# Kernel optimization log

Hardware: AMD Instinct MI355X
Metric: run time of the kernel (lower is better)

The kernel has to match this reference:

```python
import jax, jax.numpy as jnp
import numpy as np

E = 64       # expert_nums
D = 32       # embed_dim
H = 4        # num_heads
HD = D // H  # head_dim = 8
B = 524288
TOP_K = 2
NOISE_EPS = 0.01


def setup_inputs() -> dict:
    key = jax.random.key(0)
    ks = jax.random.split(key, 10)
    return {
        "taskID": jax.random.randint(ks[0], (B,), 0, 6),
        "embed_table": jax.random.normal(ks[1], (6, D), jnp.float32),
        "expert_keys": jax.random.normal(ks[2], (D, D), jnp.float32),
        "in_proj_w": jax.random.normal(ks[3], (3 * D, D), jnp.float32) * 0.1,
        "in_proj_b": jax.random.normal(ks[4], (3 * D,), jnp.float32) * 0.1,
        "fc_gate_w": jax.random.normal(ks[5], (E, D), jnp.float32) * 0.1,
        "fc_gate_b": jax.random.normal(ks[6], (E,), jnp.float32) * 0.1,
        "fc_noise_w": jax.random.normal(ks[7], (E, D), jnp.float32) * 0.1,
        "fc_noise_b": jax.random.normal(ks[8], (E,), jnp.float32) * 0.1,
        "noise": jax.random.normal(ks[9], (B, E), jnp.float32),
    }


def reference(taskID, embed_table, expert_keys, in_proj_w, in_proj_b,
              fc_gate_w, fc_gate_b, fc_noise_w, fc_noise_b, noise):
    bsz = taskID.shape[0]
    x = embed_table[taskID]                                   # [B, D] task embeddings (query)
    # nn.MultiheadAttention q/k projections (v and out_proj don't affect attn_weights)
    Wq, Wk = in_proj_w[:D], in_proj_w[D:2 * D]
    bq, bk = in_proj_b[:D], in_proj_b[D:2 * D]
    Q = (x @ Wq.T + bq).reshape(bsz, H, HD)                   # [B, H, HD]
    K = (expert_keys @ Wk.T + bk).reshape(D, H, HD)           # [S=32, H, HD], shared across batch
    scores = jnp.einsum('bhd,shd->bhs', Q, K) / np.sqrt(HD).astype(np.float32)
    attn_w = jax.nn.softmax(scores, axis=-1).mean(axis=1)     # averaged over heads -> [B, 32]
    expert_weight = jax.nn.softmax(attn_w, axis=-1)           # module re-applies softmax (faithful)
    clean_logits = expert_weight @ fc_gate_w.T + fc_gate_b    # [B, E]
    noise_std = jax.nn.softplus(expert_weight @ fc_noise_w.T + fc_noise_b) + NOISE_EPS
    logits = clean_logits + noise * noise_std                 # train=True path
    top_logits, top_indices = jax.lax.top_k(logits, min(TOP_K + 1, E))
    tk_logits = top_logits[:, :TOP_K]                         # [B, TOP_K]
    tk_indices = top_indices[:, :TOP_K]
    tk_gates = jax.nn.softmax(tk_logits, axis=-1)
    rows = jnp.arange(bsz)[:, None]
    gates = jnp.zeros_like(logits).at[rows, tk_indices].set(tk_gates)  # scatter sparse gates
    load = gates.sum(axis=0)                                  # [E]
    return gates, load
```

## Files before the change

### kernel.cpp

```cpp
#include <hip/hip_runtime.h>
#include <math.h>

#define NE 64
#define NTASK 6
#define BLK 256
#define GRID 1024
#define RPI 32

__global__ void precompute_kernel(
    const float* __restrict__ embed_table,
    const float* __restrict__ expert_keys,
    const float* __restrict__ in_proj_w,
    const float* __restrict__ in_proj_b,
    const float* __restrict__ fc_gate_w,
    const float* __restrict__ fc_gate_b,
    const float* __restrict__ fc_noise_w,
    const float* __restrict__ fc_noise_b,
    float*   __restrict__ tab_f,
    double2* __restrict__ tab_d,
    float*   __restrict__ load)
{
    __shared__ double Ksh[32][32];
    __shared__ double Qsh[6][32];
    __shared__ double sc[24][32];
    __shared__ double attn[6][32];
    __shared__ double ew[6][32];
    __shared__ double red[24];
    __shared__ double red2[6];
    const int tid = threadIdx.x;

    if (tid < NE) load[tid] = 0.f;

    for (int idx = tid; idx < 32 * 32; idx += BLK) {
        int s = idx >> 5, j = idx & 31;
        double acc = (double)in_proj_b[32 + j];
        for (int d = 0; d < 32; ++d)
            acc += (double)expert_keys[s * 32 + d] * (double)in_proj_w[(32 + j) * 32 + d];
        Ksh[s][j] = acc;
    }
    for (int idx = tid; idx < NTASK * 32; idx += BLK) {
        int t = idx >> 5, j = idx & 31;
        double acc = (double)in_proj_b[j];
        for (int d = 0; d < 32; ++d)
            acc += (double)embed_table[t * 32 + d] * (double)in_proj_w[j * 32 + d];
        Qsh[t][j] = acc;
    }
    __syncthreads();

    const double SCALE = 1.0 / (double)((float)2.8284271247461903);
    for (int idx = tid; idx < 24 * 32; idx += BLK) {
        int th = idx >> 5, s = idx & 31;
        int t = th >> 2, h = th & 3;
        double acc = 0.0;
        for (int d = 0; d < 8; ++d)
            acc += Qsh[t][h * 8 + d] * Ksh[s][h * 8 + d];
        sc[th][s] = acc * SCALE;
    }
    __syncthreads();
    if (tid < 24) {
        double m = sc[tid][0];
        for (int s = 1; s < 32; ++s) m = fmax(m, sc[tid][s]);
        red[tid] = m;
    }
    __syncthreads();
    for (int idx = tid; idx < 24 * 32; idx += BLK) {
        int th = idx >> 5, s = idx & 31;
        sc[th][s] = exp(sc[th][s] - red[th]);
    }
    __syncthreads();
    if (tid < 24) {
        double sum = 0.0;
        for (int s = 0; s < 32; ++s) sum += sc[tid][s];
        red[tid] = 1.0 / sum;
    }
    __syncthreads();
    for (int idx = tid; idx < NTASK * 32; idx += BLK) {
        int t = idx >> 5, s = idx & 31;
        attn[t][s] = 0.25 * (sc[t*4+0][s]*red[t*4+0] + sc[t*4+1][s]*red[t*4+1]
                           + sc[t*4+2][s]*red[t*4+2] + sc[t*4+3][s]*red[t*4+3]);
    }
    __syncthreads();
    if (tid < NTASK) {
        double m = attn[tid][0];
        for (int s = 1; s < 32; ++s) m = fmax(m, attn[tid][s]);
        red2[tid] = m;
    }
    __syncthreads();
    for (int idx = tid; idx < NTASK * 32; idx += BLK) {
        int t = idx >> 5, s = idx & 31;
        ew[t][s] = exp(attn[t][s] - red2[t]);
    }
    __syncthreads();
    if (tid < NTASK) {
        double sum = 0.0;
        for (int s = 0; s < 32; ++s) sum += ew[tid][s];
        red2[tid] = 1.0 / sum;
    }
    __syncthreads();

    for (int idx = tid; idx < NTASK * NE; idx += BLK) {
        int t = idx >> 6, e = idx & 63;
        double inv = red2[t];
        double a  = (double)fc_gate_b[e];
        double n0 = (double)fc_noise_b[e];
        for (int d = 0; d < 32; ++d) {
            double w = ew[t][d] * inv;
            a  += w * (double)fc_gate_w [e * 32 + d];
            n0 += w * (double)fc_noise_w[e * 32 + d];
        }
        double sp = (n0 > 0.0) ? (n0 + log1p(exp(-n0))) : log1p(exp(n0));
        double ns = sp + 0.01;
        const int o = t * 64 + e;
        tab_f[o * 2 + 0] = (float)a;
        tab_f[o * 2 + 1] = (float)ns;
        tab_d[o] = make_double2(a, ns);
    }
    for (int idx = tid; idx < 512; idx += BLK) {
        if ((idx >> 6) >= NTASK) {
            tab_f[idx * 2 + 0] = 0.f;
            tab_f[idx * 2 + 1] = 0.f;
            tab_d[idx] = make_double2(0.0, 0.0);
        }
    }
}

__global__ __launch_bounds__(BLK) void router_kernel(
    const int*     __restrict__ taskID,
    const float4*  __restrict__ noise4,
    const float4*  __restrict__ tabf4,
    const double2* __restrict__ tabd,
    float4* __restrict__ gates4,
    float*  __restrict__ load,
    int B)
{
    __shared__ float4  s_tabf4[256];
    __shared__ double2 s_tabd[512];
    __shared__ float   s_load[NE];

    const int tid = threadIdx.x;
    for (int i = tid; i < 256; i += BLK) {
        const int tt = i >> 5, cc = (i >> 3) & 3, rr = i & 7;
        const int dst = (i & ~7) | (rr ^ ((2 * cc + tt) & 7));
        s_tabf4[dst] = tabf4[i];
    }
    for (int i = tid; i < 512; i += BLK) s_tabd[i] = tabd[i];
    if (tid < NE) s_load[tid] = 0.f;
    __syncthreads();

    const int lane  = tid & 63;
    const int sub   = lane >> 2;
    const int c     = lane & 3;
    const int ebase = c * 16;
    const int W = (blockIdx.x * BLK + tid) >> 6;
    const int nWaves = GRID * (BLK / 64);
    const int nGroup = (B + RPI - 1) / RPI;

    int   tcA = 0, tcB = 0;
    float4 a0, a1, a2, a3, a4, a5, a6, a7;
    a0=a1=a2=a3=a4=a5=a6=a7 = make_float4(0.f,0.f,0.f,0.f);
    bool okA = false, okB = false;
    int  rowA = 0, rowB = 0;

    if (W < nGroup) {
        rowA = W * RPI + sub;       okA = rowA < B;
        rowB = W * RPI + 16 + sub;  okB = rowB < B;
        if (okA) {
            tcA = taskID[rowA];
            const int nb = rowA * 16 + c * 4;
            a0 = noise4[nb+0]; a1 = noise4[nb+1]; a2 = noise4[nb+2]; a3 = noise4[nb+3];
        }
        if (okB) {
            tcB = taskID[rowB];
            const int nb = rowB * 16 + c * 4;
            a4 = noise4[nb+0]; a5 = noise4[nb+1]; a6 = noise4[nb+2]; a7 = noise4[nb+3];
        }
    }

    for (int g = W; g < nGroup; g += nWaves) {
        const int gn = g + nWaves;
        int   tnA = 0, tnB = 0;
        float4 b0, b1, b2, b3, b4, b5, b6, b7;
        b0=b1=b2=b3=b4=b5=b6=b7 = make_float4(0.f,0.f,0.f,0.f);
        bool oknA = false, oknB = false;
        int  rownA = 0, rownB = 0;
        if (gn < nGroup) {
            rownA = gn * RPI + sub;       oknA = rownA < B;
            rownB = gn * RPI + 16 + sub;  oknB = rownB < B;
            if (oknA) {
                tnA = taskID[rownA];
                const int nb = rownA * 16 + c * 4;
                b0 = noise4[nb+0]; b1 = noise4[nb+1]; b2 = noise4[nb+2]; b3 = noise4[nb+3];
            }
            if (oknB) {
                tnB = taskID[rownB];
                const int nb = rownB * 16 + c * 4;
                b4 = noise4[nb+0]; b5 = noise4[nb+1]; b6 = noise4[nb+2]; b7 = noise4[nb+3];
            }
        }

#define INS(l_, e_, n_) {                                                      \
        const bool b1_ = (l_) > v1, b2_ = (l_) > v2, b3_ = (l_) > v3;          \
        v3 = b2_ ? v2 : (b3_ ? (l_) : v3);                                     \
        i3 = b2_ ? i2 : (b3_ ? (e_) : i3);                                     \
        n3 = b2_ ? n2 : (b3_ ? (n_) : n3);                                     \
        v2 = b1_ ? v1 : (b2_ ? (l_) : v2);                                     \
        i2 = b1_ ? i1 : (b2_ ? (e_) : i2);                                     \
        n2 = b1_ ? n1 : (b2_ ? (n_) : n2);                                     \
        v1 = b1_ ? (l_) : v1;                                                  \
        i1 = b1_ ? (e_) : i1;                                                  \
        n1 = b1_ ? (n_) : n1; }

#define STEP(r_, nlo_, nhi_) {                                                 \
        const float4 tv = s_tabf4[tb + ((r_) ^ x)];                            \
        const float l0 = __fadd_rn(tv.x, __fmul_rn((nlo_), tv.y));             \
        const float l1 = __fadd_rn(tv.z, __fmul_rn((nhi_), tv.w));             \
        INS(l0, ebase + 2 * (r_),     (nlo_));                                 \
        INS(l1, ebase + 2 * (r_) + 1, (nhi_)); }

#define PROCESS(t_, ok_, row_, z0, z1, z2, z3)                                 \
    {                                                                          \
        const int t  = (t_);                                                   \
        const int x  = (2 * c + t) & 7;                                        \
        const int tb = t * 32 + c * 8;                                         \
        float v1 = -INFINITY, v2 = -INFINITY, v3 = -INFINITY;                  \
        int   i1 = 0, i2 = 0, i3 = 0;                                          \
        float n1 = 0.f, n2 = 0.f, n3 = 0.f;                                    \
        STEP(0, z0.x, z0.y); STEP(1, z0.z, z0.w);                              \
        STEP(2, z1.x, z1.y); STEP(3, z1.z, z1.w);                              \
        STEP(4, z2.x, z2.y); STEP(5, z2.z, z2.w);                              \
        STEP(6, z3.x, z3.y); STEP(7, z3.z, z3.w);                              \
        _Pragma("unroll")                                                      \
        for (int m = 1; m <= 2; m <<= 1) {                                     \
            const float w1 = __shfl_xor(v1, m), w2 = __shfl_xor(v2, m), w3 = __shfl_xor(v3, m); \
            const int   j1 = __shfl_xor(i1, m), j2 = __shfl_xor(i2, m), j3 = __shfl_xor(i3, m); \
            const float q1 = __shfl_xor(n1, m), q2 = __shfl_xor(n2, m), q3 = __shfl_xor(n3, m); \
            const bool aw = (v1 > w1) || (v1 == w1 && i1 < j1);                \
            const float p1 = aw ? v1 : w1, p2 = aw ? v2 : w2, p3 = aw ? v3 : w3; \
            const int   pi1 = aw ? i1 : j1, pi2 = aw ? i2 : j2, pi3 = aw ? i3 : j3; \
            const float pn1 = aw ? n1 : q1, pn2 = aw ? n2 : q2, pn3 = aw ? n3 : q3; \
            const float u1 = aw ? w1 : v1, u2 = aw ? w2 : v2;                  \
            const int   ui1 = aw ? j1 : i1, ui2 = aw ? j2 : i2;                \
            const float un1 = aw ? q1 : n1, un2 = aw ? q2 : n2;                \
            const bool b2 = (p2 > u1) || (p2 == u1 && pi2 < ui1);              \
            const bool b3a = (p3 > u1) || (p3 == u1 && pi3 < ui1);             \
            const bool b3b = (p2 > u2) || (p2 == u2 && pi2 < ui2);             \
            v1 = p1;  i1 = pi1; n1 = pn1;                                      \
            v2 = b2 ? p2 : u1;  i2 = b2 ? pi2 : ui1;  n2 = b2 ? pn2 : un1;     \
            v3 = b2 ? (b3a ? p3 : u1) : (b3b ? p2 : u2);                       \
            i3 = b2 ? (b3a ? pi3 : ui1) : (b3b ? pi2 : ui2);                   \
            n3 = b2 ? (b3a ? pn3 : un1) : (b3b ? pn2 : un2);                   \
        }                                                                      \
        const double2 A  = s_tabd[t * 64 + i1];                                \
        const double2 Bt = s_tabd[t * 64 + i2];                                \
        const double2 Ct = s_tabd[t * 64 + i3];                                \
        double da = A.x  + (double)n1 * A.y;  int ia = i1;                     \
        double db = Bt.x + (double)n2 * Bt.y; int ib = i2;                     \
        double dc = Ct.x + (double)n3 * Ct.y; int ic = i3;                     \
        if (db > da || (db == da && ib < ia)) { double tv = da; da = db; db = tv; int ti = ia; ia = ib; ib = ti; } \
        if (dc > da || (dc == da && ic < ia)) { double tv = da; da = dc; dc = tv; int ti = ia; ia = ic; ic = ti; } \
        if (dc > db || (dc == db && ic < ib)) { double tv = db; db = dc; dc = tv; int ti = ib; ib = ic; ic = ti; } \
        const float e2 = expf((float)(db - da));                               \
        const float g1 = 1.0f / (1.0f + e2);                                   \
        const float g2 = e2 / (1.0f + e2);                                     \
        if (ok_) {                                                             \
            const int nb = (row_) * 16 + c * 4;                                \
            _Pragma("unroll")                                                  \
            for (int k = 0; k < 4; ++k) {                                      \
                const int e0 = ebase + 4 * k;                                  \
                float4 w;                                                      \
                w.x = (e0 + 0 == ia) ? g1 : ((e0 + 0 == ib) ? g2 : 0.f);       \
                w.y = (e0 + 1 == ia) ? g1 : ((e0 + 1 == ib) ? g2 : 0.f);       \
                w.z = (e0 + 2 == ia) ? g1 : ((e0 + 2 == ib) ? g2 : 0.f);       \
                w.w = (e0 + 3 == ia) ? g1 : ((e0 + 3 == ib) ? g2 : 0.f);       \
                gates4[nb + k] = w;                                            \
            }                                                                  \
            if (c == 0) {                                                      \
                atomicAdd(&s_load[ia], g1);                                    \
                atomicAdd(&s_load[ib], g2);                                    \
            }                                                                  \
        }                                                                      \
    }

        PROCESS(tcA, okA, rowA, a0, a1, a2, a3)
        PROCESS(tcB, okB, rowB, a4, a5, a6, a7)

#undef PROCESS
#undef STEP
#undef INS

        tcA = tnA; rowA = rownA; okA = oknA;
        tcB = tnB; rowB = rownB; okB = oknB;
        a0 = b0; a1 = b1; a2 = b2; a3 = b3;
        a4 = b4; a5 = b5; a6 = b6; a7 = b7;
    }
    __syncthreads();
    if (tid < NE) atomicAdd(&load[tid], s_load[tid]);
}

extern "C" void kernel_launch(void* const* d_in, const int* in_sizes, int n_in,
                              void* d_out, int out_size, void* d_ws, size_t ws_size,
                              hipStream_t stream) {
    const int*   taskID      = (const int*)  d_in[0];
    const float* embed_table = (const float*)d_in[1];
    const float* expert_keys = (const float*)d_in[2];
    const float* in_proj_w   = (const float*)d_in[3];
    const float* in_proj_b   = (const float*)d_in[4];
    const float* fc_gate_w   = (const float*)d_in[5];
    const float* fc_gate_b   = (const float*)d_in[6];
    const float* fc_noise_w  = (const float*)d_in[7];
    const float* fc_noise_b  = (const float*)d_in[8];
    const float* noise       = (const float*)d_in[9];

    const int B = in_sizes[0];

    float*   tab_f = (float*)d_ws;
    double2* tab_d = (double2*)((char*)d_ws + 4096);

    float* gates = (float*)d_out;
    float* load  = gates + (size_t)B * NE;

    precompute_kernel<<<1, BLK, 0, stream>>>(embed_table, expert_keys, in_proj_w, in_proj_b,
                                             fc_gate_w, fc_gate_b, fc_noise_w, fc_noise_b,
                                             tab_f, tab_d, load);

    router_kernel<<<GRID, BLK, 0, stream>>>(taskID, (const float4*)noise,
                                            (const float4*)tab_f, tab_d,
                                            (float4*)gates, load, B);
}
```

Before: 114.5 us.

## Fuse table precompute into router kernel, recomputing per block

```diff
diff --git a/kernel.cpp b/kernel.cpp
--- a/kernel.cpp
+++ b/kernel.cpp
@@ -7,19 +7,24 @@
 #define GRID 1024
 #define RPI 32
 
-__global__ void precompute_kernel(
-    const float* __restrict__ embed_table,
-    const float* __restrict__ expert_keys,
-    const float* __restrict__ in_proj_w,
-    const float* __restrict__ in_proj_b,
-    const float* __restrict__ fc_gate_w,
-    const float* __restrict__ fc_gate_b,
-    const float* __restrict__ fc_noise_w,
-    const float* __restrict__ fc_noise_b,
-    float*   __restrict__ tab_f,
-    double2* __restrict__ tab_d,
-    float*   __restrict__ load)
+__global__ __launch_bounds__(BLK) void router_kernel(
+    const int*     __restrict__ taskID,
+    const float4*  __restrict__ noise4,
+    const float*   __restrict__ embed_table,
+    const float*   __restrict__ expert_keys,
+    const float*   __restrict__ in_proj_w,
+    const float*   __restrict__ in_proj_b,
+    const float*   __restrict__ fc_gate_w,
+    const float*   __restrict__ fc_gate_b,
+    const float*   __restrict__ fc_noise_w,
+    const float*   __restrict__ fc_noise_b,
+    float4* __restrict__ gates4,
+    float*  __restrict__ load,
+    int B)
 {
+    __shared__ float4  s_tabf4[256];
+    __shared__ double2 s_tabd[512];
+    __shared__ float   s_load[NE];
     __shared__ double Ksh[32][32];
     __shared__ double Qsh[6][32];
     __shared__ double sc[24][32];
@@ -27,9 +32,8 @@
     __shared__ double ew[6][32];
     __shared__ double red[24];
     __shared__ double red2[6];
+
     const int tid = threadIdx.x;
-
-    if (tid < NE) load[tid] = 0.f;
 
     for (int idx = tid; idx < 32 * 32; idx += BLK) {
         int s = idx >> 5, j = idx & 31;
@@ -98,52 +102,28 @@
     }
     __syncthreads();
 
-    for (int idx = tid; idx < NTASK * NE; idx += BLK) {
-        int t = idx >> 6, e = idx & 63;
-        double inv = red2[t];
-        double a  = (double)fc_gate_b[e];
-        double n0 = (double)fc_noise_b[e];
-        for (int d = 0; d < 32; ++d) {
-            double w = ew[t][d] * inv;
-            a  += w * (double)fc_gate_w [e * 32 + d];
-            n0 += w * (double)fc_noise_w[e * 32 + d];
+    {
+        float2* s_tabf2 = (float2*)s_tabf4;
+        for (int idx = tid; idx < NTASK * NE; idx += BLK) {
+            int t = idx >> 6, e = idx & 63;
+            double inv = red2[t];
+            double a  = (double)fc_gate_b[e];
+            double n0 = (double)fc_noise_b[e];
+            for (int d = 0; d < 32; ++d) {
+                double w = ew[t][d] * inv;
+                a  += w * (double)fc_gate_w [e * 32 + d];
+                n0 += w * (double)fc_noise_w[e * 32 + d];
+            }
+            double sp = (n0 > 0.0) ? (n0 + log1p(exp(-n0))) : log1p(exp(n0));
+            double ns = sp + 0.01;
+            const int p  = e >> 1;
+            const int cc = (p >> 3) & 3, rr = p & 7;
+            const int i4 = t * 32 + p;
+            const int dst = (i4 & ~7) | (rr ^ ((2 * cc + t) & 7));
+            s_tabf2[dst * 2 + (e & 1)] = make_float2((float)a, (float)ns);
+            s_tabd[t * 64 + e] = make_double2(a, ns);
         }
-        double sp = (n0 > 0.0) ? (n0 + log1p(exp(-n0))) : log1p(exp(n0));
-        double ns = sp + 0.01;
-        const int o = t * 64 + e;
-        tab_f[o * 2 + 0] = (float)a;
-        tab_f[o * 2 + 1] = (float)ns;
-        tab_d[o] = make_double2(a, ns);
-    }
-    for (int idx = tid; idx < 512; idx += BLK) {
-        if ((idx >> 6) >= NTASK) {
-            tab_f[idx * 2 + 0] = 0.f;
-            tab_f[idx * 2 + 1] = 0.f;
-            tab_d[idx] = make_double2(0.0, 0.0);
-        }
-    }
-}
-
-__global__ __launch_bounds__(BLK) void router_kernel(
-    const int*     __restrict__ taskID,
-    const float4*  __restrict__ noise4,
-    const float4*  __restrict__ tabf4,
-    const double2* __restrict__ tabd,
-    float4* __restrict__ gates4,
-    float*  __restrict__ load,
-    int B)
-{
-    __shared__ float4  s_tabf4[256];
-    __shared__ double2 s_tabd[512];
-    __shared__ float   s_load[NE];
-
-    const int tid = threadIdx.x;
-    for (int i = tid; i < 256; i += BLK) {
-        const int tt = i >> 5, cc = (i >> 3) & 3, rr = i & 7;
-        const int dst = (i & ~7) | (rr ^ ((2 * cc + tt) & 7));
-        s_tabf4[dst] = tabf4[i];
-    }
-    for (int i = tid; i < 512; i += BLK) s_tabd[i] = tabd[i];
+    }
     if (tid < NE) s_load[tid] = 0.f;
     __syncthreads();
 
@@ -313,17 +293,13 @@
 
     const int B = in_sizes[0];
 
-    float*   tab_f = (float*)d_ws;
-    double2* tab_d = (double2*)((char*)d_ws + 4096);
-
     float* gates = (float*)d_out;
     float* load  = gates + (size_t)B * NE;
 
-    precompute_kernel<<<1, BLK, 0, stream>>>(embed_table, expert_keys, in_proj_w, in_proj_b,
-                                             fc_gate_w, fc_gate_b, fc_noise_w, fc_noise_b,
-                                             tab_f, tab_d, load);
+    hipMemsetAsync(load, 0, NE * sizeof(float), stream);
 
     router_kernel<<<GRID, BLK, 0, stream>>>(taskID, (const float4*)noise,
-                                            (const float4*)tab_f, tab_d,
+                                            embed_table, expert_keys, in_proj_w, in_proj_b,
+                                            fc_gate_w, fc_gate_b, fc_noise_w, fc_noise_b,
                                             (float4*)gates, load, B);
 }
```

New measurement: 135.7 us. 1.19x slower.

## Track top-2 instead of top-3 and write gates via zero-fill plus scatter

Applied to the files above, without the earlier changes.

```diff
diff --git a/kernel.cpp b/kernel.cpp
--- a/kernel.cpp
+++ b/kernel.cpp
@@ -20,6 +20,12 @@
     double2* __restrict__ tab_d,
     float*   __restrict__ load)
 {
+    __shared__ float s_win[96 * 32];
+    __shared__ float s_wg[64 * 32];
+    __shared__ float s_wn[64 * 32];
+    __shared__ float s_keys[32 * 32];
+    __shared__ float s_emb[6 * 32];
+    __shared__ float s_bin[96], s_bg[64], s_bn[64];
     __shared__ double Ksh[32][32];
     __shared__ double Qsh[6][32];
     __shared__ double sc[24][32];
@@ -31,18 +37,26 @@
 
     if (tid < NE) load[tid] = 0.f;
 
+    for (int i = tid; i < 96 * 32; i += BLK) s_win[i] = in_proj_w[i];
+    for (int i = tid; i < 64 * 32; i += BLK) { s_wg[i] = fc_gate_w[i]; s_wn[i] = fc_noise_w[i]; }
+    for (int i = tid; i < 32 * 32; i += BLK) s_keys[i] = expert_keys[i];
+    for (int i = tid; i < 6 * 32;  i += BLK) s_emb[i] = embed_table[i];
+    if (tid < 96) s_bin[tid] = in_proj_b[tid];
+    if (tid < 64) { s_bg[tid] = fc_gate_b[tid]; s_bn[tid] = fc_noise_b[tid]; }
+    __syncthreads();
+
     for (int idx = tid; idx < 32 * 32; idx += BLK) {
         int s = idx >> 5, j = idx & 31;
-        double acc = (double)in_proj_b[32 + j];
+        double acc = (double)s_bin[32 + j];
         for (int d = 0; d < 32; ++d)
-            acc += (double)expert_keys[s * 32 + d] * (double)in_proj_w[(32 + j) * 32 + d];
+            acc += (double)s_keys[s * 32 + d] * (double)s_win[(32 + j) * 32 + d];
         Ksh[s][j] = acc;
     }
     for (int idx = tid; idx < NTASK * 32; idx += BLK) {
         int t = idx >> 5, j = idx & 31;
-        double acc = (double)in_proj_b[j];
+        double acc = (double)s_bin[j];
         for (int d = 0; d < 32; ++d)
-            acc += (double)embed_table[t * 32 + d] * (double)in_proj_w[j * 32 + d];
+            acc += (double)s_emb[t * 32 + d] * (double)s_win[j * 32 + d];
         Qsh[t][j] = acc;
     }
     __syncthreads();
@@ -98,28 +112,29 @@
     }
     __syncthreads();
 
-    for (int idx = tid; idx < NTASK * NE; idx += BLK) {
-        int t = idx >> 6, e = idx & 63;
-        double inv = red2[t];
-        double a  = (double)fc_gate_b[e];
-        double n0 = (double)fc_noise_b[e];
-        for (int d = 0; d < 32; ++d) {
-            double w = ew[t][d] * inv;
-            a  += w * (double)fc_gate_w [e * 32 + d];
-            n0 += w * (double)fc_noise_w[e * 32 + d];
-        }
-        double sp = (n0 > 0.0) ? (n0 + log1p(exp(-n0))) : log1p(exp(n0));
-        double ns = sp + 0.01;
-        const int o = t * 64 + e;
-        tab_f[o * 2 + 0] = (float)a;
-        tab_f[o * 2 + 1] = (float)ns;
-        tab_d[o] = make_double2(a, ns);
-    }
-    for (int idx = tid; idx < 512; idx += BLK) {
-        if ((idx >> 6) >= NTASK) {
-            tab_f[idx * 2 + 0] = 0.f;
-            tab_f[idx * 2 + 1] = 0.f;
-            tab_d[idx] = make_double2(0.0, 0.0);
+    {
+        float2* tab_f2 = (float2*)tab_f;
+        for (int idx = tid; idx < NTASK * NE; idx += BLK) {
+            int t = idx >> 6, e = idx & 63;
+            double inv = red2[t];
+            double a  = (double)s_bg[e];
+            double n0 = (double)s_bn[e];
+            for (int d = 0; d < 32; ++d) {
+                double w = ew[t][d] * inv;
+                a  += w * (double)s_wg[e * 32 + d];
+                n0 += w * (double)s_wn[e * 32 + d];
+            }
+            double sp = (n0 > 0.0) ? (n0 + log1p(exp(-n0))) : log1p(exp(n0));
+            double ns = sp + 0.01;
+            const int p  = e >> 1;
+            const int cc = (p >> 3) & 3, rr = p & 7;
+            const int i4 = t * 32 + p;
+            const int dst = (i4 & ~7) | (rr ^ ((2 * cc + t) & 7));
+            tab_f2[dst * 2 + (e & 1)] = make_float2((float)a, (float)ns);
+            tab_d[t * 64 + e] = make_double2(a, ns);
+        }
+        for (int idx = NTASK * NE + tid; idx < 512; idx += BLK) {
+            tab_f2[idx] = make_float2(0.f, 0.f);
         }
     }
 }
@@ -129,8 +144,8 @@
     const float4*  __restrict__ noise4,
     const float4*  __restrict__ tabf4,
     const double2* __restrict__ tabd,
-    float4* __restrict__ gates4,
-    float*  __restrict__ load,
+    float* __restrict__ gates,
+    float* __restrict__ load,
     int B)
 {
     __shared__ float4  s_tabf4[256];
@@ -138,11 +153,7 @@
     __shared__ float   s_load[NE];
 
     const int tid = threadIdx.x;
-    for (int i = tid; i < 256; i += BLK) {
-        const int tt = i >> 5, cc = (i >> 3) & 3, rr = i & 7;
-        const int dst = (i & ~7) | (rr ^ ((2 * cc + tt) & 7));
-        s_tabf4[dst] = tabf4[i];
-    }
+    for (int i = tid; i < 256; i += BLK) s_tabf4[i] = tabf4[i];
     for (int i = tid; i < 512; i += BLK) s_tabd[i] = tabd[i];
     if (tid < NE) s_load[tid] = 0.f;
     __syncthreads();
@@ -154,10 +165,11 @@
     const int W = (blockIdx.x * BLK + tid) >> 6;
     const int nWaves = GRID * (BLK / 64);
     const int nGroup = (B + RPI - 1) / RPI;
+    const float4 zero4 = make_float4(0.f, 0.f, 0.f, 0.f);
 
     int   tcA = 0, tcB = 0;
     float4 a0, a1, a2, a3, a4, a5, a6, a7;
-    a0=a1=a2=a3=a4=a5=a6=a7 = make_float4(0.f,0.f,0.f,0.f);
+    a0=a1=a2=a3=a4=a5=a6=a7 = zero4;
     bool okA = false, okB = false;
     int  rowA = 0, rowB = 0;
 
@@ -180,7 +192,7 @@
         const int gn = g + nWaves;
         int   tnA = 0, tnB = 0;
         float4 b0, b1, b2, b3, b4, b5, b6, b7;
-        b0=b1=b2=b3=b4=b5=b6=b7 = make_float4(0.f,0.f,0.f,0.f);
+        b0=b1=b2=b3=b4=b5=b6=b7 = zero4;
         bool oknA = false, oknB = false;
         int  rownA = 0, rownB = 0;
         if (gn < nGroup) {
@@ -198,11 +210,8 @@
             }
         }
 
-#define INS(l_, e_, n_) {                                                      \
-        const bool b1_ = (l_) > v1, b2_ = (l_) > v2, b3_ = (l_) > v3;          \
-        v3 = b2_ ? v2 : (b3_ ? (l_) : v3);                                     \
-        i3 = b2_ ? i2 : (b3_ ? (e_) : i3);                                     \
-        n3 = b2_ ? n2 : (b3_ ? (n_) : n3);                                     \
+#define INS2(l_, e_, n_) {                                                     \
+        const bool b1_ = (l_) > v1, b2_ = (l_) > v2;                           \
         v2 = b1_ ? v1 : (b2_ ? (l_) : v2);                                     \
         i2 = b1_ ? i1 : (b2_ ? (e_) : i2);                                     \
         n2 = b1_ ? n1 : (b2_ ? (n_) : n2);                                     \
@@ -214,66 +223,54 @@
         const float4 tv = s_tabf4[tb + ((r_) ^ x)];                            \
         const float l0 = __fadd_rn(tv.x, __fmul_rn((nlo_), tv.y));             \
         const float l1 = __fadd_rn(tv.z, __fmul_rn((nhi_), tv.w));             \
-        INS(l0, ebase + 2 * (r_),     (nlo_));                                 \
-        INS(l1, ebase + 2 * (r_) + 1, (nhi_)); }
+        INS2(l0, ebase + 2 * (r_),     (nlo_));                                \
+        INS2(l1, ebase + 2 * (r_) + 1, (nhi_)); }
 
 #define PROCESS(t_, ok_, row_, z0, z1, z2, z3)                                 \
     {                                                                          \
         const int t  = (t_);                                                   \
         const int x  = (2 * c + t) & 7;                                        \
         const int tb = t * 32 + c * 8;                                         \
-        float v1 = -INFINITY, v2 = -INFINITY, v3 = -INFINITY;                  \
-        int   i1 = 0, i2 = 0, i3 = 0;                                          \
-        float n1 = 0.f, n2 = 0.f, n3 = 0.f;                                    \
+        float v1 = -INFINITY, v2 = -INFINITY;                                  \
+        int   i1 = 0, i2 = 0;                                                  \
+        float n1 = 0.f, n2 = 0.f;                                              \
         STEP(0, z0.x, z0.y); STEP(1, z0.z, z0.w);                              \
         STEP(2, z1.x, z1.y); STEP(3, z1.z, z1.w);                              \
         STEP(4, z2.x, z2.y); STEP(5, z2.z, z2.w);                              \
         STEP(6, z3.x, z3.y); STEP(7, z3.z, z3.w);                              \
         _Pragma("unroll")                                                      \
         for (int m = 1; m <= 2; m <<= 1) {                                     \
-            const float w1 = __shfl_xor(v1, m), w2 = __shfl_xor(v2, m), w3 = __shfl_xor(v3, m); \
-            const int   j1 = __shfl_xor(i1, m), j2 = __shfl_xor(i2, m), j3 = __shfl_xor(i3, m); \
-            const float q1 = __shfl_xor(n1, m), q2 = __shfl_xor(n2, m), q3 = __shfl_xor(n3, m); \
+            const float w1 = __shfl_xor(v1, m), w2 = __shfl_xor(v2, m);        \
+            const int   j1 = __shfl_xor(i1, m), j2 = __shfl_xor(i2, m);        \
+            const float q1 = __shfl_xor(n1, m), q2 = __shfl_xor(n2, m);        \
             const bool aw = (v1 > w1) || (v1 == w1 && i1 < j1);                \
-            const float p1 = aw ? v1 : w1, p2 = aw ? v2 : w2, p3 = aw ? v3 : w3; \
-            const int   pi1 = aw ? i1 : j1, pi2 = aw ? i2 : j2, pi3 = aw ? i3 : j3; \
-            const float pn1 = aw ? n1 : q1, pn2 = aw ? n2 : q2, pn3 = aw ? n3 : q3; \
-            const float u1 = aw ? w1 : v1, u2 = aw ? w2 : v2;                  \
-            const int   ui1 = aw ? j1 : i1, ui2 = aw ? j2 : i2;                \
-            const float un1 = aw ? q1 : n1, un2 = aw ? q2 : n2;                \
+            const float p1 = aw ? v1 : w1, p2 = aw ? v2 : w2;                  \
+            const int   pi1 = aw ? i1 : j1, pi2 = aw ? i2 : j2;                \
+            const float pn1 = aw ? n1 : q1, pn2 = aw ? n2 : q2;                \
+            const float u1 = aw ? w1 : v1;                                     \
+            const int   ui1 = aw ? j1 : i1;                                    \
+            const float un1 = aw ? q1 : n1;                                    \
             const bool b2 = (p2 > u1) || (p2 == u1 && pi2 < ui1);              \
-            const bool b3a = (p3 > u1) || (p3 == u1 && pi3 < ui1);             \
-            const bool b3b = (p2 > u2) || (p2 == u2 && pi2 < ui2);             \
             v1 = p1;  i1 = pi1; n1 = pn1;                                      \
             v2 = b2 ? p2 : u1;  i2 = b2 ? pi2 : ui1;  n2 = b2 ? pn2 : un1;     \
-            v3 = b2 ? (b3a ? p3 : u1) : (b3b ? p2 : u2);                       \
-            i3 = b2 ? (b3a ? pi3 : ui1) : (b3b ? pi2 : ui2);                   \
-            n3 = b2 ? (b3a ? pn3 : un1) : (b3b ? pn2 : un2);                   \
         }                                                                      \
         const double2 A  = s_tabd[t * 64 + i1];                                \
         const double2 Bt = s_tabd[t * 64 + i2];                                \
-        const double2 Ct = s_tabd[t * 64 + i3];                                \
         double da = A.x  + (double)n1 * A.y;  int ia = i1;                     \
         double db = Bt.x + (double)n2 * Bt.y; int ib = i2;                     \
-        double dc = Ct.x + (double)n3 * Ct.y; int ic = i3;                     \
-        if (db > da || (db == da && ib < ia)) { double tv = da; da = db; db = tv; int ti = ia; ia = ib; ib = ti; } \
-        if (dc > da || (dc == da && ic < ia)) { double tv = da; da = dc; dc = tv; int ti = ia; ia = ic; ic = ti; } \
-        if (dc > db || (dc == db && ic < ib)) { double tv = db; db = dc; dc = tv; int ti = ib; ib = ic; ic = ti; } \
+        if (db > da || (db == da && ib < ia)) {                                \
+            double tv_ = da; da = db; db = tv_;                                \
+            int ti_ = ia; ia = ib; ib = ti_;                                   \
+        }                                                                      \
         const float e2 = expf((float)(db - da));                               \
         const float g1 = 1.0f / (1.0f + e2);                                   \
         const float g2 = e2 / (1.0f + e2);                                     \
         if (ok_) {                                                             \
-            const int nb = (row_) * 16 + c * 4;                                \
-            _Pragma("unroll")                                                  \
-            for (int k = 0; k < 4; ++k) {                                      \
-                const int e0 = ebase + 4 * k;                                  \
-                float4 w;                                                      \
-                w.x = (e0 + 0 == ia) ? g1 : ((e0 + 0 == ib) ? g2 : 0.f);       \
-                w.y = (e0 + 1 == ia) ? g1 : ((e0 + 1 == ib) ? g2 : 0.f);       \
-                w.z = (e0 + 2 == ia) ? g1 : ((e0 + 2 == ib) ? g2 : 0.f);       \
-                w.w = (e0 + 3 == ia) ? g1 : ((e0 + 3 == ib) ? g2 : 0.f);       \
-                gates4[nb + k] = w;                                            \
-            }                                                                  \
+            float* grow = gates + (size_t)(row_) * 64;                         \
+            float4* g4 = reinterpret_cast<float4*>(grow + ebase);              \
+            g4[0] = zero4; g4[1] = zero4; g4[2] = zero4; g4[3] = zero4;        \
+            if ((ia >> 4) == c) grow[ia] = g1;                                 \
+            if ((ib >> 4) == c) grow[ib] = g2;                                 \
             if (c == 0) {                                                      \
                 atomicAdd(&s_load[ia], g1);                                    \
                 atomicAdd(&s_load[ib], g2);                                    \
@@ -286,7 +283,7 @@
 
 #undef PROCESS
 #undef STEP
-#undef INS
+#undef INS2
 
         tcA = tnA; rowA = rownA; okA = oknA;
         tcB = tnB; rowB = rownB; okB = oknB;
@@ -325,5 +322,5 @@
 
     router_kernel<<<GRID, BLK, 0, stream>>>(taskID, (const float4*)noise,
                                             (const float4*)tab_f, tab_d,
-                                            (float4*)gates, load, B);
+                                            gates, load, B);
 }
```

Measured after the change: 117.7 us. 1.03x slower.
